# Kernel tuning notes

Measured on AMD Instinct MI355X. Metric: run time of the kernel, lower is better.

The kernel has to match this reference:

```python
import jax, jax.numpy as jnp
import numpy as np

B, IMG, TXT = 1, 2048, 256
D_MODEL = 2048
HEADS, HEAD_DIM = 16, 128
INNER = HEADS * HEAD_DIM
EPS = 1e-5
SCALE = HEAD_DIM ** -0.5


def _rmsnorm(x, w):
    # normalize over last dim (head_dim)
    return (x * jax.lax.rsqrt(jnp.mean(x * x, axis=-1, keepdims=True) + EPS)) * w


def _rope(x, cos, sin):
    # x: (B, S, H, D); cos/sin: (S, D) with pairwise-repeated freqs (interleaved convention)
    c = cos[None, :, None, :]
    s = sin[None, :, None, :]
    x1 = x[..., 0::2]
    x2 = x[..., 1::2]
    rot = jnp.stack([-x2, x1], axis=-1).reshape(x.shape)
    return x * c + rot * s


def setup_inputs() -> dict:
    key = jax.random.key(0)
    ks = jax.random.split(key, 12)
    sc_in = D_MODEL ** -0.5
    sc_inner = INNER ** -0.5
    inp = {
        'hidden_states': jax.random.normal(ks[0], (B, IMG, D_MODEL), jnp.float32),
        'encoder_hidden_states': jax.random.normal(ks[1], (B, TXT, D_MODEL), jnp.float32),
    }
    # RoPE tables over the joint (text + image) sequence, interleaved pair layout
    pos = jnp.arange(TXT + IMG, dtype=jnp.float32)
    inv = 1.0 / (10000.0 ** (jnp.arange(0, HEAD_DIM, 2, dtype=jnp.float32) / HEAD_DIM))
    freqs = pos[:, None] * inv[None, :]
    freqs = jnp.repeat(freqs, 2, axis=-1)  # (S, HEAD_DIM)
    inp['freqs_cos'] = jnp.cos(freqs)
    inp['freqs_sin'] = jnp.sin(freqs)
    # parameters (stored (in, out))
    inp['Wqkv'] = jax.random.normal(ks[2], (D_MODEL, 3 * INNER), jnp.float32) * sc_in
    inp['Wqkv_add'] = jax.random.normal(ks[3], (D_MODEL, 3 * INNER), jnp.float32) * sc_in
    inp['b_qkv_add'] = jax.random.normal(ks[4], (3 * INNER,), jnp.float32) * 0.01
    inp['norm_q_w'] = jnp.ones((HEAD_DIM,), jnp.float32)
    inp['norm_k_w'] = jnp.ones((HEAD_DIM,), jnp.float32)
    inp['norm_aq_w'] = jnp.ones((HEAD_DIM,), jnp.float32)
    inp['norm_ak_w'] = jnp.ones((HEAD_DIM,), jnp.float32)
    inp['Wout'] = jax.random.normal(ks[5], (INNER, D_MODEL), jnp.float32) * sc_inner
    inp['b_out'] = jax.random.normal(ks[6], (D_MODEL,), jnp.float32) * 0.01
    inp['Wadd_out'] = jax.random.normal(ks[7], (INNER, D_MODEL), jnp.float32) * sc_inner
    inp['b_add_out'] = jax.random.normal(ks[8], (D_MODEL,), jnp.float32) * 0.01
    return inp


def reference(hidden_states, encoder_hidden_states, freqs_cos, freqs_sin,
              Wqkv, Wqkv_add, b_qkv_add, norm_q_w, norm_k_w, norm_aq_w, norm_ak_w,
              Wout, b_out, Wadd_out, b_add_out):
    b, s_img, _ = hidden_states.shape
    s_txt = encoder_hidden_states.shape[1]

    # fused QKV projection (image stream), chunk q/k/v, unflatten heads
    qkv = hidden_states @ Wqkv  # (B, IMG, 3*INNER)
    q, k, v = jnp.split(qkv, 3, axis=-1)
    q = _rmsnorm(q.reshape(b, s_img, HEADS, HEAD_DIM), norm_q_w)
    k = _rmsnorm(k.reshape(b, s_img, HEADS, HEAD_DIM), norm_k_w)
    v = v.reshape(b, s_img, HEADS, HEAD_DIM)

    # fused QKV projection (text stream, with bias)
    eqkv = encoder_hidden_states @ Wqkv_add + b_qkv_add
    eq, ek, ev = jnp.split(eqkv, 3, axis=-1)
    eq = _rmsnorm(eq.reshape(b, s_txt, HEADS, HEAD_DIM), norm_aq_w)
    ek = _rmsnorm(ek.reshape(b, s_txt, HEADS, HEAD_DIM), norm_ak_w)
    ev = ev.reshape(b, s_txt, HEADS, HEAD_DIM)

    # joint [text; image] concatenation, then RoPE on joint Q/K
    jq = jnp.concatenate([eq, q], axis=1)
    jk = jnp.concatenate([ek, k], axis=1)
    jv = jnp.concatenate([ev, v], axis=1)
    jq = _rope(jq, freqs_cos, freqs_sin)
    jk = _rope(jk, freqs_cos, freqs_sin)

    # non-causal scaled dot-product attention, layout (B, S, H, D)
    scores = jnp.einsum('bqhd,bkhd->bhqk', jq, jk) * SCALE
    probs = jax.nn.softmax(scores, axis=-1)
    out = jnp.einsum('bhqk,bkhd->bqhd', probs, jv)  # (B, S_joint, H, D)
    out = out.reshape(b, s_txt + s_img, INNER)

    enc_out = out[:, :s_txt]
    img_out = out[:, s_txt:]
    img_out = img_out @ Wout + b_out
    enc_out = enc_out @ Wadd_out + b_add_out
    return (img_out, enc_out)
```

## Files before the change

kernel.cpp:

```cpp
#include <hip/hip_runtime.h>
#include <stdint.h>

#define HEADS 16
#define HD 128
#define S_TXT 256
#define S_IMG 2048
#define S_ALL 2304
#define DMODEL 2048
#define N_QKV 6144
#define INNER 2048
#define ATT_EPS 1e-5f
#define ATT_SCALE 0.08838834764831845f
#define LOG2E 1.4426950408889634f
#define MBOUND 16.5f
#define QT_N 18
#define TPS 36

typedef __attribute__((ext_vector_type(8))) __bf16 bf16x8;
typedef __attribute__((ext_vector_type(4))) float f32x4;
typedef __attribute__((ext_vector_type(4))) uint32_t u32x4;

__device__ __forceinline__ uint16_t f2bf(float f) {
  union { float f; uint32_t u; } v; v.f = f;
  uint32_t r = (v.u + 0x7FFF + ((v.u >> 16) & 1)) >> 16;
  return (uint16_t)r;
}
__device__ __forceinline__ float bf2f(uint16_t h) {
  union { float f; uint32_t u; } v; v.u = ((uint32_t)h) << 16;
  return v.f;
}
__device__ __forceinline__ float fexp2(float x) {
#if __has_builtin(__builtin_amdgcn_exp2f)
  return __builtin_amdgcn_exp2f(x);
#else
  return __expf(x * 0.69314718055994531f);
#endif
}

__device__ __forceinline__ void async_cp16(const void* g, void* l) {
  __builtin_amdgcn_global_load_lds(
      (const __attribute__((address_space(1))) void*)g,
      (__attribute__((address_space(3))) void*)l, 16, 0, 0);
}

__global__ __launch_bounds__(256) void k_cvt(const float* __restrict__ src,
                                             uint16_t* __restrict__ dst, int n4) {
  int i = blockIdx.x * 256 + threadIdx.x;
  int stride = gridDim.x * 256;
  for (; i < n4; i += stride) {
    float4 v = ((const float4*)src)[i];
    uint16_t o[4];
    o[0] = f2bf(v.x); o[1] = f2bf(v.y); o[2] = f2bf(v.z); o[3] = f2bf(v.w);
    ((uint2*)dst)[i] = *(const uint2*)o;
  }
}

__global__ __launch_bounds__(256) void k_cvt_t4(
    const float* __restrict__ s0, uint16_t* __restrict__ d0,
    const float* __restrict__ s1, uint16_t* __restrict__ d1,
    const float* __restrict__ s2, uint16_t* __restrict__ d2,
    const float* __restrict__ s3, uint16_t* __restrict__ d3) {
  __shared__ float t[64][65];
  int b = blockIdx.x;
  const float* src; uint16_t* dst; int R, C, tb;
  if (b < 3072)      { src = s0; dst = d0; R = DMODEL; C = N_QKV;  tb = b; }
  else if (b < 6144) { src = s1; dst = d1; R = DMODEL; C = N_QKV;  tb = b - 3072; }
  else if (b < 7168) { src = s2; dst = d2; R = INNER;  C = DMODEL; tb = b - 6144; }
  else               { src = s3; dst = d3; R = INNER;  C = DMODEL; tb = b - 7168; }
  int ntr = R >> 6;
  int tr = tb % ntr, tc = tb / ntr;
  int tid = threadIdx.x;
  int rr = tid >> 4, c4 = (tid & 15) * 4;
#pragma unroll
  for (int j = 0; j < 4; ++j) {
    int r = rr + j * 16;
    float4 v = *(const float4*)&src[(size_t)(tr * 64 + r) * C + tc * 64 + c4];
    *(float4*)&t[r][c4] = v;
  }
  __syncthreads();
  int cc = tid >> 4, r4 = (tid & 15) * 4;
#pragma unroll
  for (int j = 0; j < 4; ++j) {
    int c = cc + j * 16;
    uint16_t ov[4];
    ov[0] = f2bf(t[r4 + 0][c]); ov[1] = f2bf(t[r4 + 1][c]);
    ov[2] = f2bf(t[r4 + 2][c]); ov[3] = f2bf(t[r4 + 3][c]);
    *(uint2*)&dst[(size_t)(tc * 64 + c) * R + tr * 64 + r4] = *(const uint2*)ov;
  }
}

__global__ __launch_bounds__(512, 1) void k_gemm2(
    const uint16_t* __restrict__ A0, const uint16_t* __restrict__ B0,
    const float* __restrict__ bias0, uint16_t* __restrict__ C0,
    const uint16_t* __restrict__ A1, const uint16_t* __restrict__ B1,
    const float* __restrict__ bias1, uint16_t* __restrict__ C1,
    int seg0_tiles, int N, int K) {
  __shared__ __align__(16) char lds[3 * 49152];
  int bn = blockIdx.x, bm = blockIdx.y;
  const uint16_t* A; const uint16_t* B; const float* bias; uint16_t* C; int mrow;
  if (bm < seg0_tiles) { A = A0; B = B0; bias = bias0; C = C0; mrow = bm * 256; }
  else { A = A1; B = B1; bias = bias1; C = C1; mrow = (bm - seg0_tiles) * 256; }
  int tid = threadIdx.x, lane = tid & 63, w = tid >> 6;
  int g = lane >> 4, li = lane & 15;
  int wm = w >> 1, wn = w & 1;
  const int NKI = K / 64;

  int rowin = lane >> 3;
  int csrc = (lane & 7) ^ rowin;

  auto stage = [&](int t, char* buf) {
    int kt = t * 64;
#pragma unroll
    for (int j = 0; j < 4; ++j) {
      int r = w * 4 + j;
      int tr = r * 8 + rowin;
      async_cp16(A + (size_t)(mrow + tr) * K + kt + 8 * csrc, buf + r * 1024);
    }
#pragma unroll
    for (int j = 0; j < 2; ++j) {
      int r = w * 2 + j;
      int tr = r * 8 + rowin;
      async_cp16(B + (size_t)(bn * 128 + tr) * K + kt + 8 * csrc, buf + 32768 + r * 1024);
    }
  };

  f32x4 acc[4][4] = {};

  stage(0, lds);
  stage(1, lds + 49152);
  asm volatile("s_waitcnt vmcnt(6)" ::: "memory");
  __builtin_amdgcn_s_barrier();
  asm volatile("" ::: "memory");

  int cbuf = 0, sbuf = 2;
  for (int t = 0; t < NKI; ++t) {
    const char* cur = lds + cbuf * 49152;
    if (t + 2 < NKI) stage(t + 2, lds + sbuf * 49152);

    bf16x8 af[2][4], bfv[2][4];
#pragma unroll
    for (int kk = 0; kk < 2; ++kk) {
#pragma unroll
      for (int mi = 0; mi < 4; ++mi) {
        int row = wm * 64 + mi * 16 + li;
        int ch = (kk * 4 + g) ^ (row & 7);
        af[kk][mi] = __builtin_bit_cast(bf16x8, *(const u32x4*)(cur + row * 128 + ch * 16));
      }
#pragma unroll
      for (int ni = 0; ni < 4; ++ni) {
        int row = wn * 64 + ni * 16 + li;
        int ch = (kk * 4 + g) ^ (row & 7);
        bfv[kk][ni] = __builtin_bit_cast(bf16x8, *(const u32x4*)(cur + 32768 + row * 128 + ch * 16));
      }
    }
    __builtin_amdgcn_s_setprio(1);
#pragma unroll
    for (int kk = 0; kk < 2; ++kk)
#pragma unroll
      for (int mi = 0; mi < 4; ++mi)
#pragma unroll
        for (int ni = 0; ni < 4; ++ni)
          acc[mi][ni] = __builtin_amdgcn_mfma_f32_16x16x32_bf16(af[kk][mi], bfv[kk][ni], acc[mi][ni], 0, 0, 0);
    __builtin_amdgcn_s_setprio(0);

    if (t + 1 < NKI) {
      if (t + 2 < NKI) asm volatile("s_waitcnt vmcnt(6)" ::: "memory");
      else             asm volatile("s_waitcnt vmcnt(0)" ::: "memory");
      __builtin_amdgcn_s_barrier();
      asm volatile("" ::: "memory");
    }
    cbuf = (cbuf + 1 == 3) ? 0 : cbuf + 1;
    sbuf = (sbuf + 1 == 3) ? 0 : sbuf + 1;
  }

#pragma unroll
  for (int mi = 0; mi < 4; ++mi) {
#pragma unroll
    for (int ni = 0; ni < 4; ++ni) {
      int col = bn * 128 + wn * 64 + ni * 16 + li;
      float bv = bias ? bias[col] : 0.0f;
#pragma unroll
      for (int i = 0; i < 4; ++i) {
        int r = mrow + wm * 64 + mi * 16 + 4 * g + i;
        C[(size_t)r * N + col] = f2bf(acc[mi][ni][i] + bv);
      }
    }
  }
}

__global__ __launch_bounds__(256, 4) void k_gemmO(
    const uint16_t* __restrict__ A0, const uint16_t* __restrict__ B0,
    const float* __restrict__ bias0, float* __restrict__ C0,
    const uint16_t* __restrict__ A1, const uint16_t* __restrict__ B1,
    const float* __restrict__ bias1, float* __restrict__ C1,
    int seg0_tiles, int N, int K) {
  __shared__ __align__(16) char lds[4 * 8192];
  int bn = blockIdx.x, bm = blockIdx.y;
  const uint16_t* A; const uint16_t* B; const float* bias; float* C; int mrow;
  if (bm < seg0_tiles) { A = A0; B = B0; bias = bias0; C = C0; mrow = bm * 128; }
  else { A = A1; B = B1; bias = bias1; C = C1; mrow = (bm - seg0_tiles) * 128; }
  int tid = threadIdx.x, lane = tid & 63, w = tid >> 6;
  int g = lane >> 4, li = lane & 15;
  int wm = w >> 1, wn = w & 1;
  const int NKT = K / 32;

  int rowin = lane >> 2;
  int csrc = (lane & 3) ^ (rowin & 3);

  auto stage = [&](int t, int buf) {
    int kt = t * 32;
#pragma unroll
    for (int j = 0; j < 2; ++j) {
      int r = w * 2 + j;
      int tr = r * 16 + rowin;
      async_cp16(A + (size_t)(mrow + tr) * K + kt + 8 * csrc, lds + buf * 8192 + r * 1024);
    }
#pragma unroll
    for (int j = 0; j < 2; ++j) {
      int r = w * 2 + j;
      int tr = r * 16 + rowin;
      async_cp16(B + (size_t)(bn * 128 + tr) * K + kt + 8 * csrc, lds + 16384 + buf * 8192 + r * 1024);
    }
  };

  f32x4 acc[4][4] = {};
  stage(0, 0);
  asm volatile("s_waitcnt vmcnt(0)" ::: "memory");
  __builtin_amdgcn_s_barrier();
  asm volatile("" ::: "memory");

  for (int t = 0; t < NKT; ++t) {
    int cur = t & 1;
    bool pre = (t + 1 < NKT);
    if (pre) stage(t + 1, cur ^ 1);
    const char* Ac = lds + cur * 8192;
    const char* Bc = lds + 16384 + cur * 8192;

    bf16x8 af[4], bfv[4];
#pragma unroll
    for (int mi = 0; mi < 4; ++mi) {
      int row = wm * 64 + mi * 16 + li;
      af[mi] = __builtin_bit_cast(bf16x8, *(const u32x4*)(Ac + row * 64 + (g ^ (row & 3)) * 16));
    }
#pragma unroll
    for (int ni = 0; ni < 4; ++ni) {
      int row = wn * 64 + ni * 16 + li;
      bfv[ni] = __builtin_bit_cast(bf16x8, *(const u32x4*)(Bc + row * 64 + (g ^ (row & 3)) * 16));
    }
    __builtin_amdgcn_s_setprio(1);
#pragma unroll
    for (int mi = 0; mi < 4; ++mi)
#pragma unroll
      for (int ni = 0; ni < 4; ++ni)
        acc[mi][ni] = __builtin_amdgcn_mfma_f32_16x16x32_bf16(af[mi], bfv[ni], acc[mi][ni], 0, 0, 0);
    __builtin_amdgcn_s_setprio(0);

    if (pre) asm volatile("s_waitcnt vmcnt(0)" ::: "memory");
    __builtin_amdgcn_s_barrier();
    asm volatile("" ::: "memory");
  }

#pragma unroll
  for (int mi = 0; mi < 4; ++mi) {
#pragma unroll
    for (int ni = 0; ni < 4; ++ni) {
      int col = bn * 128 + wn * 64 + ni * 16 + li;
      float bv = bias[col];
#pragma unroll
      for (int i = 0; i < 4; ++i) {
        int r = mrow + wm * 64 + mi * 16 + 4 * g + i;
        C[(size_t)r * N + col] = acc[mi][ni][i] + bv;
      }
    }
  }
}

__global__ __launch_bounds__(256) void k_post(
    const uint16_t* __restrict__ qkv_img, const uint16_t* __restrict__ qkv_txt,
    const float* __restrict__ fcos, const float* __restrict__ fsin,
    const float* __restrict__ wq, const float* __restrict__ wk,
    const float* __restrict__ waq, const float* __restrict__ wak,
    uint16_t* __restrict__ Qo, uint16_t* __restrict__ Ko) {
  int s = blockIdx.x;
  const uint16_t* row = (s < S_TXT) ? qkv_txt + (size_t)s * N_QKV
                                    : qkv_img + (size_t)(s - S_TXT) * N_QKV;
  const float* wqp = (s < S_TXT) ? waq : wq;
  const float* wkp = (s < S_TXT) ? wak : wk;
  int tid = threadIdx.x, lane = tid & 63, w = tid >> 6;
  int h = w * 4 + (lane >> 4);
  int d0 = (lane & 15) * 8;
  float cs[8], sn[8];
#pragma unroll
  for (int j = 0; j < 8; ++j) {
    cs[j] = fcos[s * HD + d0 + j];
    sn[j] = fsin[s * HD + d0 + j];
  }
#pragma unroll
  for (int part = 0; part < 2; ++part) {
    const uint16_t* src = row + part * INNER + h * HD + d0;
    u32x4 raw = *(const u32x4*)src;
    const uint16_t* rp = (const uint16_t*)&raw;
    float x[8], ss = 0.f;
#pragma unroll
    for (int j = 0; j < 8; ++j) { x[j] = bf2f(rp[j]); ss += x[j] * x[j]; }
    ss += __shfl_xor(ss, 1); ss += __shfl_xor(ss, 2);
    ss += __shfl_xor(ss, 4); ss += __shfl_xor(ss, 8);
    float rn = rsqrtf(ss * (1.0f / HD) + ATT_EPS);
    const float* wp = part ? wkp : wqp;
#pragma unroll
    for (int j = 0; j < 8; ++j) x[j] = x[j] * rn * wp[d0 + j];
    float y[8];
#pragma unroll
    for (int j = 0; j < 8; j += 2) {
      y[j]     = x[j] * cs[j] - x[j + 1] * sn[j];
      y[j + 1] = x[j + 1] * cs[j + 1] + x[j] * sn[j + 1];
    }
    float sc = part ? 1.0f : (ATT_SCALE * LOG2E);
    uint16_t ov[8];
#pragma unroll
    for (int j = 0; j < 8; ++j) ov[j] = f2bf(y[j] * sc);
    uint16_t* dst = (part ? Ko : Qo) + ((size_t)h * S_ALL + s) * HD + d0;
    *(u32x4*)dst = *(const u32x4*)ov;
  }
}

__global__ __launch_bounds__(256) void k_vt(
    const uint16_t* __restrict__ qkv_img, const uint16_t* __restrict__ qkv_txt,
    uint16_t* __restrict__ VTo) {
  __shared__ uint16_t Vl[64][136];
  int st = blockIdx.x % 36, h = blockIdx.x / 36;
  int s0 = st * 64;
  const uint16_t* base = (s0 < S_TXT) ? qkv_txt + (size_t)s0 * N_QKV
                                      : qkv_img + (size_t)(s0 - S_TXT) * N_QKV;
  base += 2 * INNER + h * HD;
  int tid = threadIdx.x;
#pragma unroll
  for (int it = 0; it < 4; ++it) {
    int idx = it * 256 + tid;
    int r = idx >> 4, c = idx & 15;
    *(u32x4*)&Vl[r][c * 8] = *(const u32x4*)(base + (size_t)r * N_QKV + c * 8);
  }
  __syncthreads();
#pragma unroll
  for (int it = 0; it < 4; ++it) {
    int idx = it * 256 + tid;
    int d = idx >> 3, sc = (idx & 7) * 8;
    uint16_t tmp[8];
#pragma unroll
    for (int j = 0; j < 8; ++j) tmp[j] = Vl[sc + j][d];
    *(u32x4*)&VTo[((size_t)h * HD + d) * S_ALL + s0 + sc] = *(const u32x4*)tmp;
  }
}

__global__ __launch_bounds__(256, 3) void k_attn(
    const uint16_t* __restrict__ Qg, const uint16_t* __restrict__ Kg,
    const uint16_t* __restrict__ VTg,
    float* __restrict__ part0, float* __restrict__ part1,
    float* __restrict__ lsumP) {
  __shared__ __align__(16) char Kt[2][8192];
  __shared__ __align__(16) char Vt[2][8192];
  __shared__ __align__(16) uint16_t Pl[4][32 * 40];

  int b0 = blockIdx.x;
  int bid = (b0 & 7) * 72 + (b0 >> 3);
  int h = bid / 36, r6 = bid % 36, sp = r6 / 18, qt = r6 % 18;
  int tid = threadIdx.x, lane = tid & 63, w = tid >> 6;
  int g = lane >> 4, li = lane & 15;

  const uint16_t* Kh = Kg + (size_t)h * S_ALL * HD;
  const uint16_t* Vh = VTg + (size_t)h * HD * S_ALL;
  float* po = (sp ? part1 : part0) + ((size_t)(h * QT_N + qt) * 128 + w * 32) * 128;

  int qbase = qt * 128 + w * 32;
  bf16x8 qf[2][4];
#pragma unroll
  for (int q2 = 0; q2 < 2; ++q2) {
    const uint16_t* qp = Qg + ((size_t)h * S_ALL + qbase + q2 * 16 + li) * HD;
#pragma unroll
    for (int kc = 0; kc < 4; ++kc)
      qf[q2][kc] = __builtin_bit_cast(bf16x8, *(const u32x4*)(qp + kc * 32 + g * 8));
  }
  f32x4 o[2][8] = {};
  float lsum[2] = {0.f, 0.f};

  auto stage = [&](int tk, int buf) {
#pragma unroll
    for (int j = 0; j < 2; ++j) {
      int cj = w * 128 + j * 64 + lane;
      int row = cj >> 4, c = (cj & 15) ^ (row & 15);
      async_cp16(Kh + (size_t)(tk * 32 + row) * HD + 8 * c, Kt[buf] + (w * 128 + j * 64) * 16);
    }
#pragma unroll
    for (int j = 0; j < 2; ++j) {
      int cj = w * 128 + j * 64 + lane;
      int row = cj >> 2, c = (cj & 3) ^ ((row >> 1) & 3);
      async_cp16(Vh + (size_t)row * S_ALL + tk * 32 + 8 * c, Vt[buf] + (w * 128 + j * 64) * 16);
    }
  };

  int t0 = sp * TPS;
  stage(t0, 0);
  asm volatile("s_waitcnt vmcnt(0)" ::: "memory");
  __builtin_amdgcn_s_barrier();
  asm volatile("" ::: "memory");

  for (int t = 0; t < TPS; ++t) {
    int cur = t & 1;
    if (t + 1 < TPS) stage(t0 + t + 1, cur ^ 1);
    const char* KtC = Kt[cur];
    const char* VtC = Vt[cur];

    f32x4 sc[2][2];
#pragma unroll
    for (int q2 = 0; q2 < 2; ++q2)
#pragma unroll
      for (int kb = 0; kb < 2; ++kb)
        sc[q2][kb] = (f32x4){-MBOUND, -MBOUND, -MBOUND, -MBOUND};
    __builtin_amdgcn_s_setprio(1);
#pragma unroll
    for (int kb = 0; kb < 2; ++kb)
#pragma unroll
      for (int kc = 0; kc < 4; ++kc) {
        int ch = (kc * 4 + g) ^ li;
        bf16x8 kf = __builtin_bit_cast(bf16x8,
            *(const u32x4*)(KtC + (kb * 16 + li) * 256 + ch * 16));
        sc[0][kb] = __builtin_amdgcn_mfma_f32_16x16x32_bf16(kf, qf[0][kc], sc[0][kb], 0, 0, 0);
        sc[1][kb] = __builtin_amdgcn_mfma_f32_16x16x32_bf16(kf, qf[1][kc], sc[1][kb], 0, 0, 0);
      }
    __builtin_amdgcn_s_setprio(0);

    uint16_t* Pw = &Pl[w][0];
#pragma unroll
    for (int q2 = 0; q2 < 2; ++q2)
#pragma unroll
      for (int kb = 0; kb < 2; ++kb) {
        float p0 = fexp2(sc[q2][kb][0]);
        float p1 = fexp2(sc[q2][kb][1]);
        float p2 = fexp2(sc[q2][kb][2]);
        float p3 = fexp2(sc[q2][kb][3]);
        lsum[q2] += (p0 + p1) + (p2 + p3);
        uint2 pk;
        pk.x = (uint32_t)f2bf(p0) | ((uint32_t)f2bf(p1) << 16);
        pk.y = (uint32_t)f2bf(p2) | ((uint32_t)f2bf(p3) << 16);
        *(uint2*)((char*)Pw + (q2 * 16 + li) * 80 + kb * 32 + g * 8) = pk;
      }

    bf16x8 pf[2];
#pragma unroll
    for (int q2 = 0; q2 < 2; ++q2)
      pf[q2] = __builtin_bit_cast(bf16x8,
          *(const u32x4*)((const char*)Pw + (q2 * 16 + li) * 80 + g * 16));
    __builtin_amdgcn_s_setprio(1);
#pragma unroll
    for (int db = 0; db < 8; ++db) {
      int vrow = db * 16 + li;
      int ch = g ^ ((vrow >> 1) & 3);
      bf16x8 vf = __builtin_bit_cast(bf16x8, *(const u32x4*)(VtC + vrow * 64 + ch * 16));
      o[0][db] = __builtin_amdgcn_mfma_f32_16x16x32_bf16(pf[0], vf, o[0][db], 0, 0, 0);
      o[1][db] = __builtin_amdgcn_mfma_f32_16x16x32_bf16(pf[1], vf, o[1][db], 0, 0, 0);
    }
    __builtin_amdgcn_s_setprio(0);

    asm volatile("s_waitcnt vmcnt(0)" ::: "memory");
    __builtin_amdgcn_s_barrier();
    asm volatile("" ::: "memory");
  }

#pragma unroll
  for (int q2 = 0; q2 < 2; ++q2) {
    float v = lsum[q2];
    v += __shfl_xor(v, 16);
    v += __shfl_xor(v, 32);
    lsum[q2] = v;
  }
  if (lane < 16) {
#pragma unroll
    for (int q2 = 0; q2 < 2; ++q2)
      lsumP[((size_t)sp * HEADS + h) * S_ALL + qbase + q2 * 16 + lane] = lsum[q2];
  }
#pragma unroll
  for (int q2 = 0; q2 < 2; ++q2)
#pragma unroll
    for (int db = 0; db < 8; ++db)
#pragma unroll
      for (int i = 0; i < 4; ++i)
        po[(q2 * 16 + 4 * g + i) * 128 + db * 16 + li] = o[q2][db][i];
}

__global__ __launch_bounds__(256) void k_comb(
    const float* __restrict__ p0, const float* __restrict__ p1,
    const float* __restrict__ lsumP, uint16_t* __restrict__ attn) {
  int q = blockIdx.x, qt = q >> 7, ql = q & 127;
#pragma unroll
  for (int rep = 0; rep < 2; ++rep) {
    int d4 = threadIdx.x + rep * 256;
    int d = d4 * 4, h = d >> 7, dl = d & 127;
    size_t off = (((size_t)h * QT_N + qt) * 128 + ql) * 128 + dl;
    float4 a = *(const float4*)&p0[off];
    float4 b = *(const float4*)&p1[off];
    float l0 = lsumP[(size_t)h * S_ALL + q];
    float l1 = lsumP[((size_t)HEADS + h) * S_ALL + q];
    float inv = 1.0f / (l0 + l1);
    uint16_t ov[4];
    ov[0] = f2bf((a.x + b.x) * inv); ov[1] = f2bf((a.y + b.y) * inv);
    ov[2] = f2bf((a.z + b.z) * inv); ov[3] = f2bf((a.w + b.w) * inv);
    *(uint2*)&attn[(size_t)q * INNER + d] = *(const uint2*)ov;
  }
}

extern "C" void kernel_launch(void* const* d_in, const int* in_sizes, int n_in,
                              void* d_out, int out_size, void* d_ws, size_t ws_size,
                              hipStream_t stream) {
  const float* hidden = (const float*)d_in[0];
  const float* enc    = (const float*)d_in[1];
  const float* fcos   = (const float*)d_in[2];
  const float* fsin   = (const float*)d_in[3];
  const float* Wqkv   = (const float*)d_in[4];
  const float* Wqkva  = (const float*)d_in[5];
  const float* bqkva  = (const float*)d_in[6];
  const float* nqw    = (const float*)d_in[7];
  const float* nkw    = (const float*)d_in[8];
  const float* naqw   = (const float*)d_in[9];
  const float* nakw   = (const float*)d_in[10];
  const float* Wout   = (const float*)d_in[11];
  const float* bout   = (const float*)d_in[12];
  const float* Wadd   = (const float*)d_in[13];
  const float* badd   = (const float*)d_in[14];
  float* out_img = (float*)d_out;
  float* out_enc = (float*)d_out + (size_t)S_IMG * DMODEL;

  char* ws = (char*)d_ws;
  size_t off = 0;
  auto alloc = [&](size_t bytes) {
    char* p = ws + off;
    off += (bytes + 255) & ~(size_t)255;
    return p;
  };
  uint16_t* hs_bf   = (uint16_t*)alloc((size_t)S_IMG * DMODEL * 2);
  uint16_t* enc_bf  = (uint16_t*)alloc((size_t)S_TXT * DMODEL * 2);
  char*     wqkv_base = alloc((size_t)N_QKV * DMODEL * 2 * 2);
  uint16_t* WqkvT   = (uint16_t*)wqkv_base;
  uint16_t* WqkvaT  = (uint16_t*)(wqkv_base + (size_t)N_QKV * DMODEL * 2);
  uint16_t* WoutT   = (uint16_t*)alloc((size_t)DMODEL * INNER * 2);
  uint16_t* WaddT   = (uint16_t*)alloc((size_t)DMODEL * INNER * 2);
  uint16_t* qkv_img = (uint16_t*)alloc((size_t)S_IMG * N_QKV * 2);
  uint16_t* qkv_txt = (uint16_t*)alloc((size_t)S_TXT * N_QKV * 2);
  uint16_t* Qb   = (uint16_t*)wqkv_base;
  uint16_t* Kb   = Qb + (size_t)HEADS * S_ALL * HD;
  uint16_t* VTb  = Kb + (size_t)HEADS * S_ALL * HD;
  uint16_t* attn = VTb + (size_t)HEADS * S_ALL * HD;
  float* part0 = (float*)d_out;
  float* part1 = (float*)qkv_img;
  float* lsumP = (float*)enc_bf;

  k_cvt<<<1024, 256, 0, stream>>>(hidden, hs_bf, S_IMG * DMODEL / 4);
  k_cvt<<<256, 256, 0, stream>>>(enc, enc_bf, S_TXT * DMODEL / 4);
  k_cvt_t4<<<8192, 256, 0, stream>>>(Wqkv, WqkvT, Wqkva, WqkvaT, Wout, WoutT, Wadd, WaddT);

  dim3 gq(N_QKV / 128, (S_TXT + S_IMG) / 256);
  k_gemm2<<<gq, 512, 0, stream>>>(enc_bf, WqkvaT, bqkva, qkv_txt,
                                  hs_bf, WqkvT, nullptr, qkv_img,
                                  1, N_QKV, DMODEL);

  k_post<<<S_ALL, 256, 0, stream>>>(qkv_img, qkv_txt, fcos, fsin,
                                    nqw, nkw, naqw, nakw, Qb, Kb);
  k_vt<<<36 * HEADS, 256, 0, stream>>>(qkv_img, qkv_txt, VTb);

  k_attn<<<HEADS * QT_N * 2, 256, 0, stream>>>(Qb, Kb, VTb, part0, part1, lsumP);
  k_comb<<<S_ALL, 256, 0, stream>>>(part0, part1, lsumP, attn);

  dim3 go(DMODEL / 128, S_ALL / 128);
  k_gemmO<<<go, 256, 0, stream>>>(attn, WaddT, badd, out_enc,
                                  attn + (size_t)S_TXT * INNER, WoutT, bout, out_img,
                                  2, DMODEL, DMODEL);
}
```

Measured before the change: 235.6 us.

## Drop attention split-KV combine pass and shrink QKV GEMM k-tile

The attention kernel no longer splits the key sequence in two with a separate combine kernel. Each block now walks all 72 key tiles and writes normalized bf16 output directly, which removes the fp32 partial writes and reads and one launch. In exchange the attention grid halves to 288 blocks, which may underfill the GPU. Separately, the QKV GEMM k-tile drops from 64 to 32, cutting LDS use from 144KB to 72KB, and launch bounds are raised to allow more occupancy, at the cost of more barriers per unit of K.

```diff
diff --git a/kernel.cpp b/kernel.cpp
--- a/kernel.cpp
+++ b/kernel.cpp
@@ -14,7 +14,7 @@
 #define LOG2E 1.4426950408889634f
 #define MBOUND 16.5f
 #define QT_N 18
-#define TPS 36
+#define NT32 72
 
 typedef __attribute__((ext_vector_type(8))) __bf16 bf16x8;
 typedef __attribute__((ext_vector_type(4))) float f32x4;
@@ -89,13 +89,13 @@
   }
 }
 
-__global__ __launch_bounds__(512, 1) void k_gemm2(
+__global__ __launch_bounds__(512, 4) void k_gemm2(
     const uint16_t* __restrict__ A0, const uint16_t* __restrict__ B0,
     const float* __restrict__ bias0, uint16_t* __restrict__ C0,
     const uint16_t* __restrict__ A1, const uint16_t* __restrict__ B1,
     const float* __restrict__ bias1, uint16_t* __restrict__ C1,
     int seg0_tiles, int N, int K) {
-  __shared__ __align__(16) char lds[3 * 49152];
+  __shared__ __align__(16) char lds[3 * 24576];
   int bn = blockIdx.x, bm = blockIdx.y;
   const uint16_t* A; const uint16_t* B; const float* bias; uint16_t* C; int mrow;
   if (bm < seg0_tiles) { A = A0; B = B0; bias = bias0; C = C0; mrow = bm * 256; }
@@ -103,69 +103,62 @@
   int tid = threadIdx.x, lane = tid & 63, w = tid >> 6;
   int g = lane >> 4, li = lane & 15;
   int wm = w >> 1, wn = w & 1;
-  const int NKI = K / 64;
-
-  int rowin = lane >> 3;
-  int csrc = (lane & 7) ^ rowin;
+  const int NKI = K / 32;
 
   auto stage = [&](int t, char* buf) {
-    int kt = t * 64;
-#pragma unroll
-    for (int j = 0; j < 4; ++j) {
-      int r = w * 4 + j;
-      int tr = r * 8 + rowin;
-      async_cp16(A + (size_t)(mrow + tr) * K + kt + 8 * csrc, buf + r * 1024);
-    }
-#pragma unroll
-    for (int j = 0; j < 2; ++j) {
-      int r = w * 2 + j;
-      int tr = r * 8 + rowin;
-      async_cp16(B + (size_t)(bn * 128 + tr) * K + kt + 8 * csrc, buf + 32768 + r * 1024);
+    int kt = t * 32;
+    {
+      int cj = w * 64 + lane;
+      int row = cj >> 2, c = (cj & 3) ^ ((row >> 1) & 3);
+      async_cp16(A + (size_t)(mrow + row) * K + kt + 8 * c, buf + w * 1024);
+      cj += 512; row = cj >> 2; c = (cj & 3) ^ ((row >> 1) & 3);
+      async_cp16(A + (size_t)(mrow + row) * K + kt + 8 * c, buf + 8192 + w * 1024);
+    }
+    {
+      int cj = w * 64 + lane;
+      int row = cj >> 2, c = (cj & 3) ^ ((row >> 1) & 3);
+      async_cp16(B + (size_t)(bn * 128 + row) * K + kt + 8 * c, buf + 16384 + w * 1024);
     }
   };
 
   f32x4 acc[4][4] = {};
 
   stage(0, lds);
-  stage(1, lds + 49152);
-  asm volatile("s_waitcnt vmcnt(6)" ::: "memory");
+  stage(1, lds + 24576);
+  asm volatile("s_waitcnt vmcnt(3)" ::: "memory");
   __builtin_amdgcn_s_barrier();
   asm volatile("" ::: "memory");
 
   int cbuf = 0, sbuf = 2;
   for (int t = 0; t < NKI; ++t) {
-    const char* cur = lds + cbuf * 49152;
-    if (t + 2 < NKI) stage(t + 2, lds + sbuf * 49152);
-
-    bf16x8 af[2][4], bfv[2][4];
-#pragma unroll
-    for (int kk = 0; kk < 2; ++kk) {
-#pragma unroll
-      for (int mi = 0; mi < 4; ++mi) {
-        int row = wm * 64 + mi * 16 + li;
-        int ch = (kk * 4 + g) ^ (row & 7);
-        af[kk][mi] = __builtin_bit_cast(bf16x8, *(const u32x4*)(cur + row * 128 + ch * 16));
-      }
-#pragma unroll
-      for (int ni = 0; ni < 4; ++ni) {
-        int row = wn * 64 + ni * 16 + li;
-        int ch = (kk * 4 + g) ^ (row & 7);
-        bfv[kk][ni] = __builtin_bit_cast(bf16x8, *(const u32x4*)(cur + 32768 + row * 128 + ch * 16));
-      }
+    const char* cur = lds + cbuf * 24576;
+    bool pre = (t + 2 < NKI);
+    if (pre) stage(t + 2, lds + sbuf * 24576);
+
+    bf16x8 af[4], bfv[4];
+#pragma unroll
+    for (int mi = 0; mi < 4; ++mi) {
+      int row = wm * 64 + mi * 16 + li;
+      int ch = g ^ ((row >> 1) & 3);
+      af[mi] = __builtin_bit_cast(bf16x8, *(const u32x4*)(cur + row * 64 + ch * 16));
+    }
+#pragma unroll
+    for (int ni = 0; ni < 4; ++ni) {
+      int row = wn * 64 + ni * 16 + li;
+      int ch = g ^ ((row >> 1) & 3);
+      bfv[ni] = __builtin_bit_cast(bf16x8, *(const u32x4*)(cur + 16384 + row * 64 + ch * 16));
     }
     __builtin_amdgcn_s_setprio(1);
 #pragma unroll
-    for (int kk = 0; kk < 2; ++kk)
-#pragma unroll
-      for (int mi = 0; mi < 4; ++mi)
-#pragma unroll
-        for (int ni = 0; ni < 4; ++ni)
-          acc[mi][ni] = __builtin_amdgcn_mfma_f32_16x16x32_bf16(af[kk][mi], bfv[kk][ni], acc[mi][ni], 0, 0, 0);
+    for (int mi = 0; mi < 4; ++mi)
+#pragma unroll
+      for (int ni = 0; ni < 4; ++ni)
+        acc[mi][ni] = __builtin_amdgcn_mfma_f32_16x16x32_bf16(af[mi], bfv[ni], acc[mi][ni], 0, 0, 0);
     __builtin_amdgcn_s_setprio(0);
 
     if (t + 1 < NKI) {
-      if (t + 2 < NKI) asm volatile("s_waitcnt vmcnt(6)" ::: "memory");
-      else             asm volatile("s_waitcnt vmcnt(0)" ::: "memory");
+      if (pre) asm volatile("s_waitcnt vmcnt(3)" ::: "memory");
+      else     asm volatile("s_waitcnt vmcnt(0)" ::: "memory");
       __builtin_amdgcn_s_barrier();
       asm volatile("" ::: "memory");
     }
@@ -354,22 +347,19 @@
 
 __global__ __launch_bounds__(256, 3) void k_attn(
     const uint16_t* __restrict__ Qg, const uint16_t* __restrict__ Kg,
-    const uint16_t* __restrict__ VTg,
-    float* __restrict__ part0, float* __restrict__ part1,
-    float* __restrict__ lsumP) {
+    const uint16_t* __restrict__ VTg, uint16_t* __restrict__ attn) {
   __shared__ __align__(16) char Kt[2][8192];
   __shared__ __align__(16) char Vt[2][8192];
   __shared__ __align__(16) uint16_t Pl[4][32 * 40];
 
   int b0 = blockIdx.x;
-  int bid = (b0 & 7) * 72 + (b0 >> 3);
-  int h = bid / 36, r6 = bid % 36, sp = r6 / 18, qt = r6 % 18;
+  int bid = (b0 & 7) * 36 + (b0 >> 3);
+  int h = bid / QT_N, qt = bid % QT_N;
   int tid = threadIdx.x, lane = tid & 63, w = tid >> 6;
   int g = lane >> 4, li = lane & 15;
 
   const uint16_t* Kh = Kg + (size_t)h * S_ALL * HD;
   const uint16_t* Vh = VTg + (size_t)h * HD * S_ALL;
-  float* po = (sp ? part1 : part0) + ((size_t)(h * QT_N + qt) * 128 + w * 32) * 128;
 
   int qbase = qt * 128 + w * 32;
   bf16x8 qf[2][4];
@@ -398,15 +388,14 @@
     }
   };
 
-  int t0 = sp * TPS;
-  stage(t0, 0);
+  stage(0, 0);
   asm volatile("s_waitcnt vmcnt(0)" ::: "memory");
   __builtin_amdgcn_s_barrier();
   asm volatile("" ::: "memory");
 
-  for (int t = 0; t < TPS; ++t) {
+  for (int t = 0; t < NT32; ++t) {
     int cur = t & 1;
-    if (t + 1 < TPS) stage(t0 + t + 1, cur ^ 1);
+    if (t + 1 < NT32) stage(t + 1, cur ^ 1);
     const char* KtC = Kt[cur];
     const char* VtC = Vt[cur];
 
@@ -466,17 +455,15 @@
     asm volatile("" ::: "memory");
   }
 
+  float inv[2][4];
 #pragma unroll
   for (int q2 = 0; q2 < 2; ++q2) {
     float v = lsum[q2];
     v += __shfl_xor(v, 16);
     v += __shfl_xor(v, 32);
-    lsum[q2] = v;
-  }
-  if (lane < 16) {
-#pragma unroll
-    for (int q2 = 0; q2 < 2; ++q2)
-      lsumP[((size_t)sp * HEADS + h) * S_ALL + qbase + q2 * 16 + lane] = lsum[q2];
+#pragma unroll
+    for (int i = 0; i < 4; ++i)
+      inv[q2][i] = 1.0f / __shfl(v, 4 * g + i);
   }
 #pragma unroll
   for (int q2 = 0; q2 < 2; ++q2)
@@ -484,28 +471,8 @@
     for (int db = 0; db < 8; ++db)
 #pragma unroll
       for (int i = 0; i < 4; ++i)
-        po[(q2 * 16 + 4 * g + i) * 128 + db * 16 + li] = o[q2][db][i];
-}
-
-__global__ __launch_bounds__(256) void k_comb(
-    const float* __restrict__ p0, const float* __restrict__ p1,
-    const float* __restrict__ lsumP, uint16_t* __restrict__ attn) {
-  int q = blockIdx.x, qt = q >> 7, ql = q & 127;
-#pragma unroll
-  for (int rep = 0; rep < 2; ++rep) {
-    int d4 = threadIdx.x + rep * 256;
-    int d = d4 * 4, h = d >> 7, dl = d & 127;
-    size_t off = (((size_t)h * QT_N + qt) * 128 + ql) * 128 + dl;
-    float4 a = *(const float4*)&p0[off];
-    float4 b = *(const float4*)&p1[off];
-    float l0 = lsumP[(size_t)h * S_ALL + q];
-    float l1 = lsumP[((size_t)HEADS + h) * S_ALL + q];
-    float inv = 1.0f / (l0 + l1);
-    uint16_t ov[4];
-    ov[0] = f2bf((a.x + b.x) * inv); ov[1] = f2bf((a.y + b.y) * inv);
-    ov[2] = f2bf((a.z + b.z) * inv); ov[3] = f2bf((a.w + b.w) * inv);
-    *(uint2*)&attn[(size_t)q * INNER + d] = *(const uint2*)ov;
-  }
+        attn[(size_t)(qbase + q2 * 16 + 4 * g + i) * INNER + h * HD + db * 16 + li] =
+            f2bf(o[q2][db][i] * inv[q2][i]);
 }
 
 extern "C" void kernel_launch(void* const* d_in, const int* in_sizes, int n_in,
@@ -549,9 +516,6 @@
   uint16_t* Kb   = Qb + (size_t)HEADS * S_ALL * HD;
   uint16_t* VTb  = Kb + (size_t)HEADS * S_ALL * HD;
   uint16_t* attn = VTb + (size_t)HEADS * S_ALL * HD;
-  float* part0 = (float*)d_out;
-  float* part1 = (float*)qkv_img;
-  float* lsumP = (float*)enc_bf;
 
   k_cvt<<<1024, 256, 0, stream>>>(hidden, hs_bf, S_IMG * DMODEL / 4);
   k_cvt<<<256, 256, 0, stream>>>(enc, enc_bf, S_TXT * DMODEL / 4);
@@ -566,8 +530,7 @@
                                     nqw, nkw, naqw, nakw, Qb, Kb);
   k_vt<<<36 * HEADS, 256, 0, stream>>>(qkv_img, qkv_txt, VTb);
 
-  k_attn<<<HEADS * QT_N * 2, 256, 0, stream>>>(Qb, Kb, VTb, part0, part1, lsumP);
-  k_comb<<<S_ALL, 256, 0, stream>>>(part0, part1, lsumP, attn);
+  k_attn<<<HEADS * QT_N, 256, 0, stream>>>(Qb, Kb, VTb, attn);
 
   dim3 go(DMODEL / 128, S_ALL / 128);
   k_gemmO<<<go, 256, 0, stream>>>(attn, WaddT, badd, out_enc,
```

Measured after the change: 251.8 us. 1.07x slower.
